# Kernel optimization log

Measured on AMD Instinct MI355X. Metric: run time of the kernel, lower is better.

The kernel has to match this reference:

```python
import jax, jax.numpy as jnp
import numpy as np

DIM = 1024
HEADS = 16
DIM_HEAD = 64
INNER = HEADS * DIM_HEAD
EPS_NORM = 1e-12  # F.normalize eps
LN_EPS = 1e-5     # torch F.layer_norm default eps


def setup_inputs() -> dict:
    key = jax.random.key(0)
    ks = jax.random.split(key, 6)
    x = jax.random.normal(ks[0], (8, 1024, DIM), dtype=jnp.float32)
    ln_gamma = jnp.ones((DIM,), jnp.float32)
    q_gamma = jnp.ones((HEADS, 1, DIM_HEAD), jnp.float32)
    k_gamma = jnp.ones((HEADS, 1, DIM_HEAD), jnp.float32)
    # nn.Linear default init ~ U(-1/sqrt(fan_in), 1/sqrt(fan_in))
    w_qkv = jax.random.uniform(ks[1], (DIM, 3 * INNER), jnp.float32, -1.0, 1.0) / np.sqrt(DIM)
    w_out = jax.random.uniform(ks[2], (INNER, DIM), jnp.float32, -1.0, 1.0) / np.sqrt(INNER)
    return {"x": x, "ln_gamma": ln_gamma, "q_gamma": q_gamma, "k_gamma": k_gamma,
            "w_qkv": w_qkv, "w_out": w_out}


def _layer_norm(x, gamma):
    mu = jnp.mean(x, axis=-1, keepdims=True)
    var = jnp.var(x, axis=-1, keepdims=True)
    return (x - mu) * jax.lax.rsqrt(var + LN_EPS) * gamma  # beta is zeros buffer


def _rms(x, gamma):
    # F.normalize(x, dim=-1) * sqrt(d) * gamma
    n = jnp.linalg.norm(x, axis=-1, keepdims=True)
    normed = x / jnp.maximum(n, EPS_NORM)
    return normed * (DIM_HEAD ** 0.5) * gamma


def reference(x, ln_gamma, q_gamma, k_gamma, w_qkv, w_out):
    b, n, _ = x.shape
    h, d = HEADS, DIM_HEAD
    xn = _layer_norm(x, ln_gamma)
    qkv = xn @ w_qkv  # [b, n, 3*inner]
    q, k, v = jnp.split(qkv, 3, axis=-1)
    # b n (h d) -> b h n d
    to_heads = lambda t: t.reshape(b, n, h, d).transpose(0, 2, 1, 3)
    q, k, v = to_heads(q), to_heads(k), to_heads(v)
    q = _rms(q, q_gamma)
    k = _rms(k, k_gamma)
    dots = jnp.einsum('bhid,bhjd->bhij', q, k)  # no extra scale (scale baked into RMSNorm)
    attn = jax.nn.softmax(dots, axis=-1)
    out = jnp.einsum('bhij,bhjd->bhid', attn, v)
    out = out.transpose(0, 2, 1, 3).reshape(b, n, h * d)
    return out @ w_out
```

## Files before the change

kernel.cpp:

```cpp
#include <hip/hip_runtime.h>
#include <hip/hip_bf16.h>
#include <math.h>

#define DIMX   1024
#define HEADS  16
#define DH     64
#define NB     8
#define NSEQ   1024
#define ROWS   (NB * NSEQ)
#define QKVW   (3 * DIMX)
#define LOG2E  1.44269504088896f

typedef _Float16 half8 __attribute__((ext_vector_type(8)));
typedef _Float16 half4 __attribute__((ext_vector_type(4)));
typedef float floatx4 __attribute__((ext_vector_type(4)));

#define GLD_LDS16(gptr, lptr) __builtin_amdgcn_global_load_lds( \
    (const __attribute__((address_space(1))) void*)(gptr),      \
    (__attribute__((address_space(3))) void*)(lptr), 16, 0, 0)

__device__ __forceinline__ float fexp2(float x) {
#if __has_builtin(__builtin_amdgcn_exp2f)
    return __builtin_amdgcn_exp2f(x);
#else
    return __expf(x * 0.69314718056f);
#endif
}

__global__ __launch_bounds__(256) void lnw_kernel(const float* __restrict__ x,
                                                  const float* __restrict__ gamma,
                                                  const float* __restrict__ Wq,
                                                  const float* __restrict__ Wo,
                                                  _Float16* __restrict__ xn,
                                                  _Float16* __restrict__ WqT,
                                                  _Float16* __restrict__ WoT) {
    __shared__ float tile[32][33];
    __shared__ float sbuf[4], ssbuf[4];
    int t = threadIdx.x;

    if (blockIdx.x < ROWS) {
        int row = blockIdx.x;
        const float* xr = x + (size_t)row * DIMX;
        _Float16* xo = xn + (size_t)row * DIMX;

        float4 v = ((const float4*)xr)[t];
        float s  = v.x + v.y + v.z + v.w;
        float ss = v.x*v.x + v.y*v.y + v.z*v.z + v.w*v.w;
        #pragma unroll
        for (int o = 32; o > 0; o >>= 1) {
            s  += __shfl_down(s, o);
            ss += __shfl_down(ss, o);
        }
        int lane = t & 63, wid = t >> 6;
        if (lane == 0) { sbuf[wid] = s; ssbuf[wid] = ss; }
        __syncthreads();
        if (t == 0) {
            float a = 0.f, b2 = 0.f;
            for (int i = 0; i < 4; i++) { a += sbuf[i]; b2 += ssbuf[i]; }
            sbuf[0] = a; ssbuf[0] = b2;
        }
        __syncthreads();
        float mean = sbuf[0] * (1.0f / DIMX);
        float var  = ssbuf[0] * (1.0f / DIMX) - mean * mean;
        float rstd = rsqrtf(var + 1e-5f);

        float4 g = ((const float4*)gamma)[t];
        half4 o;
        o.x = (_Float16)((v.x - mean) * rstd * g.x);
        o.y = (_Float16)((v.y - mean) * rstd * g.y);
        o.z = (_Float16)((v.z - mean) * rstd * g.z);
        o.w = (_Float16)((v.w - mean) * rstd * g.w);
        *(half4*)(xo + t * 4) = o;
    } else {
        int idx = blockIdx.x - ROWS;
        int bx = idx & 127, by = idx >> 7;
        const float* W; _Float16* WT; int N, n0;
        if (bx < 96) { W = Wq; WT = WqT; N = QKVW; n0 = bx * 32; }
        else         { W = Wo; WT = WoT; N = DIMX; n0 = (bx - 96) * 32; }
        int k0 = by * 32;
        int tx = t & 31, ty = t >> 5;
        #pragma unroll
        for (int i = 0; i < 32; i += 8)
            tile[ty + i][tx] = W[(size_t)(k0 + ty + i) * N + n0 + tx];
        __syncthreads();
        #pragma unroll
        for (int i = 0; i < 32; i += 8)
            WT[(size_t)(n0 + ty + i) * 1024 + k0 + tx] = (_Float16)tile[tx][ty + i];
    }
}

__global__ __launch_bounds__(256) void hgemm_qkv(const _Float16* __restrict__ A,
                                                 const _Float16* __restrict__ BT,
                                                 const float* __restrict__ qg,
                                                 const float* __restrict__ kg,
                                                 _Float16* __restrict__ qf,
                                                 _Float16* __restrict__ kf,
                                                 _Float16* __restrict__ vt) {
    __shared__ _Float16 As[128 * 64];
    __shared__ _Float16 Bs[128 * 64];
    const int K = DIMX;

    int t = threadIdx.x;
    int wave = t >> 6, lane = t & 63;
    int quad = lane >> 4, l16 = lane & 15;
    int wm = (wave >> 1) * 64;
    int wn = (wave & 1) * 64;
    size_t m0 = (size_t)blockIdx.y * 128, n0 = (size_t)blockIdx.x * 128;

    floatx4 acc[4][4] = {};

    int sr = t >> 3, sg = t & 7;
    int swz = sg ^ (sr & 7);
    const _Float16* ag = A  + (m0 + sr) * (size_t)K + swz * 8;
    const _Float16* bg = BT + (n0 + sr) * (size_t)K + swz * 8;
    char* lA = (char*)As + wave * 1024;
    char* lB = (char*)Bs + wave * 1024;

    for (int k0 = 0; k0 < K; k0 += 64) {
        #pragma unroll
        for (int i = 0; i < 4; i++) {
            GLD_LDS16(ag + (size_t)(i * 32) * K + k0, lA + i * 4096);
            GLD_LDS16(bg + (size_t)(i * 32) * K + k0, lB + i * 4096);
        }
        __syncthreads();

        half8 af[2][4], bf[2][4];
        #pragma unroll
        for (int kk = 0; kk < 2; kk++) {
            #pragma unroll
            for (int mf = 0; mf < 4; mf++)
                af[kk][mf] = *(const half8*)&As[(wm + mf * 16 + l16) * 64
                                 + (((kk * 4 + quad) ^ (l16 & 7)) * 8)];
            #pragma unroll
            for (int nf = 0; nf < 4; nf++)
                bf[kk][nf] = *(const half8*)&Bs[(wn + nf * 16 + l16) * 64
                                 + (((kk * 4 + quad) ^ (l16 & 7)) * 8)];
        }

        #pragma unroll
        for (int kk = 0; kk < 2; kk++)
            #pragma unroll
            for (int mf = 0; mf < 4; mf++)
                #pragma unroll
                for (int nf = 0; nf < 4; nf++)
                    acc[mf][nf] = __builtin_amdgcn_mfma_f32_16x16x32_f16(
                        bf[kk][nf], af[kk][mf], acc[mf][nf], 0, 0, 0);
        __syncthreads();
    }

    int which = (int)(n0 >> 10);
    int nloc  = ((int)n0 & 1023) + wn;
    int h = nloc >> 6;

    if (which < 2) {
        const float* g = (which == 0) ? qg : kg;
        float emul = (which == 0) ? LOG2E : 1.0f;
        _Float16* dstbuf = (which == 0) ? qf : kf;
        #pragma unroll
        for (int mf = 0; mf < 4; mf++) {
            size_t tok = m0 + wm + mf * 16 + l16;
            int b = (int)(tok >> 10), ntk = (int)(tok & 1023);
            _Float16* dst = dstbuf + (((size_t)(b * 16 + h)) * 1024 + ntk) * 64;
            float ss = 0.f;
            #pragma unroll
            for (int nf = 0; nf < 4; nf++)
                #pragma unroll
                for (int r = 0; r < 4; r++) ss += acc[mf][nf][r] * acc[mf][nf][r];
            ss += __shfl_xor(ss, 16);
            ss += __shfl_xor(ss, 32);
            float scale = 8.0f * emul / fmaxf(sqrtf(ss), 1e-12f);
            #pragma unroll
            for (int nf = 0; nf < 4; nf++) {
                half4 p;
                #pragma unroll
                for (int r = 0; r < 4; r++)
                    p[r] = (_Float16)(acc[mf][nf][r] * scale *
                                      g[h * 64 + nf * 16 + quad * 4 + r]);
                *(half4*)(dst + nf * 16 + quad * 4) = p;
            }
        }
    } else {
        #pragma unroll
        for (int mf = 0; mf < 4; mf++) {
            size_t tok = m0 + wm + mf * 16 + l16;
            int b = (int)(tok >> 10), ntk = (int)(tok & 1023);
            int nt = ntk >> 6;
            _Float16* vd = vt + ((size_t)((b * 16 + h) * 16 + nt) * 64) * 64
                              + mf * 16 + l16;
            #pragma unroll
            for (int nf = 0; nf < 4; nf++)
                #pragma unroll
                for (int r = 0; r < 4; r++)
                    vd[(size_t)(nf * 16 + quad * 4 + r) * 64] =
                        (_Float16)acc[mf][nf][r];
        }
    }
}

__global__ __launch_bounds__(256, 3) void flash_kernel(const _Float16* __restrict__ qf,
                                                       const _Float16* __restrict__ kf,
                                                       const _Float16* __restrict__ vt,
                                                       _Float16* __restrict__ obuf) {
    __shared__ _Float16 Ks[2][64 * 64];
    __shared__ _Float16 VTs[2][64 * 64];
    __shared__ _Float16 Ps[4][16][68];

    int t = threadIdx.x;
    int wave = t >> 6, lane = t & 63;
    int quad = lane >> 4, l16 = lane & 15;
    int bh = blockIdx.x & 127, qt = blockIdx.x >> 7;

    const _Float16* qb = qf + ((size_t)bh * 1024 + qt * 128) * 64;
    const _Float16* kb = kf + (size_t)bh * 65536;
    const _Float16* vb = vt + (size_t)bh * 65536;

    half8 aq[2][2];
    #pragma unroll
    for (int st = 0; st < 2; st++) {
        const _Float16* qrow = qb + (wave * 32 + st * 16 + l16) * 64;
        aq[st][0] = *(const half8*)(qrow + quad * 8);
        aq[st][1] = *(const half8*)(qrow + 32 + quad * 8);
    }

    floatx4 o[2][4] = {};
    float m_i[2] = {-INFINITY, -INFINITY};
    float l_i[2] = {0.f, 0.f};

    int sr = t >> 3;
    int sg = t & 7;
    int swz = sg ^ (sr & 7);

    #pragma unroll
    for (int i = 0; i < 2; i++) {
        GLD_LDS16(kb + (i * 32 + sr) * 64 + swz * 8, (char*)Ks[0]  + wave * 1024 + i * 4096);
        GLD_LDS16(vb + (i * 32 + sr) * 64 + swz * 8, (char*)VTs[0] + wave * 1024 + i * 4096);
    }

    for (int kt = 0; kt < 16; kt++) {
        int cur = kt & 1;
        __syncthreads();

        if (kt < 15) {
            const _Float16* kn = kb + (size_t)(kt + 1) * 4096;
            const _Float16* vn = vb + (size_t)(kt + 1) * 4096;
            #pragma unroll
            for (int i = 0; i < 2; i++) {
                GLD_LDS16(kn + (i * 32 + sr) * 64 + swz * 8,
                          (char*)Ks[cur ^ 1]  + wave * 1024 + i * 4096);
                GLD_LDS16(vn + (i * 32 + sr) * 64 + swz * 8,
                          (char*)VTs[cur ^ 1] + wave * 1024 + i * 4096);
            }
        }

        #pragma unroll
        for (int st = 0; st < 2; st++) {
            floatx4 sc[4] = {};
            #pragma unroll
            for (int kc = 0; kc < 2; kc++) {
                #pragma unroll
                for (int nf = 0; nf < 4; nf++) {
                    half8 ak = *(const half8*)&Ks[cur][(nf * 16 + l16) * 64
                                    + (((kc * 4 + quad) ^ (l16 & 7)) * 8)];
                    sc[nf] = __builtin_amdgcn_mfma_f32_16x16x32_f16(
                        ak, aq[st][kc], sc[nf], 0, 0, 0);
                }
            }

            float mx = sc[0][0];
            #pragma unroll
            for (int nf = 0; nf < 4; nf++)
                #pragma unroll
                for (int r = 0; r < 4; r++) mx = fmaxf(mx, sc[nf][r]);
            mx = fmaxf(mx, __shfl_xor(mx, 16));
            mx = fmaxf(mx, __shfl_xor(mx, 32));
            if (mx > m_i[st]) {
                float alpha = fexp2(m_i[st] - mx);
                l_i[st] *= alpha;
                #pragma unroll
                for (int nf = 0; nf < 4; nf++) o[st][nf] *= alpha;
                m_i[st] = mx;
            }
            float mcur = m_i[st];
            float psum = 0.f;
            #pragma unroll
            for (int nf = 0; nf < 4; nf++)
                #pragma unroll
                for (int r = 0; r < 4; r++) {
                    float p = fexp2(sc[nf][r] - mcur);
                    sc[nf][r] = p;
                    psum += p;
                }
            l_i[st] += psum;

            #pragma unroll
            for (int nf = 0; nf < 4; nf++) {
                half4 p4;
                #pragma unroll
                for (int r = 0; r < 4; r++) p4[r] = (_Float16)sc[nf][r];
                *(half4*)&Ps[wave][l16][nf * 16 + quad * 4] = p4;
            }

            #pragma unroll
            for (int kc = 0; kc < 2; kc++) {
                half4 p0 = *(const half4*)&Ps[wave][l16][kc * 32 + quad * 8];
                half4 p1 = *(const half4*)&Ps[wave][l16][kc * 32 + quad * 8 + 4];
                half8 bp;
                #pragma unroll
                for (int j = 0; j < 4; j++) { bp[j] = p0[j]; bp[4 + j] = p1[j]; }
                #pragma unroll
                for (int nf = 0; nf < 4; nf++) {
                    half8 av = *(const half8*)&VTs[cur][(nf * 16 + l16) * 64
                                    + (((kc * 4 + quad) ^ (l16 & 7)) * 8)];
                    o[st][nf] = __builtin_amdgcn_mfma_f32_16x16x32_f16(
                        av, bp, o[st][nf], 0, 0, 0);
                }
            }
        }
    }

    int b = bh >> 4, h = bh & 15;
    #pragma unroll
    for (int st = 0; st < 2; st++) {
        float lsum = l_i[st];
        lsum += __shfl_xor(lsum, 16);
        lsum += __shfl_xor(lsum, 32);
        float inv = 1.0f / lsum;
        size_t row = (size_t)b * NSEQ + qt * 128 + wave * 32 + st * 16 + l16;
        #pragma unroll
        for (int nf = 0; nf < 4; nf++) {
            half4 o4;
            #pragma unroll
            for (int r = 0; r < 4; r++) o4[r] = (_Float16)(o[st][nf][r] * inv);
            *(half4*)(obuf + row * 1024 + h * 64 + nf * 16 + quad * 4) = o4;
        }
    }
}

__global__ __launch_bounds__(256) void hgemm_out(const _Float16* __restrict__ A,
                                                 const _Float16* __restrict__ BT,
                                                 float* __restrict__ C) {
    __shared__ _Float16 As[128 * 64];
    __shared__ _Float16 Bs[128 * 64];
    const int K = DIMX, N = DIMX;

    int t = threadIdx.x;
    int wave = t >> 6, lane = t & 63;
    int quad = lane >> 4, l16 = lane & 15;
    int wm = (wave >> 1) * 64, wn = (wave & 1) * 64;
    size_t m0 = (size_t)blockIdx.y * 128, n0 = (size_t)blockIdx.x * 128;

    floatx4 acc[4][4] = {};

    int sr = t >> 3, sg = t & 7;
    int swz = sg ^ (sr & 7);
    const _Float16* ag = A  + (m0 + sr) * (size_t)K + swz * 8;
    const _Float16* bg = BT + (n0 + sr) * (size_t)K + swz * 8;
    char* lA = (char*)As + wave * 1024;
    char* lB = (char*)Bs + wave * 1024;

    for (int k0 = 0; k0 < K; k0 += 64) {
        #pragma unroll
        for (int i = 0; i < 4; i++) {
            GLD_LDS16(ag + (size_t)(i * 32) * K + k0, lA + i * 4096);
            GLD_LDS16(bg + (size_t)(i * 32) * K + k0, lB + i * 4096);
        }
        __syncthreads();

        half8 af[2][4], bf[2][4];
        #pragma unroll
        for (int kk = 0; kk < 2; kk++) {
            #pragma unroll
            for (int mf = 0; mf < 4; mf++)
                af[kk][mf] = *(const half8*)&As[(wm + mf * 16 + l16) * 64
                                 + (((kk * 4 + quad) ^ (l16 & 7)) * 8)];
            #pragma unroll
            for (int nf = 0; nf < 4; nf++)
                bf[kk][nf] = *(const half8*)&Bs[(wn + nf * 16 + l16) * 64
                                 + (((kk * 4 + quad) ^ (l16 & 7)) * 8)];
        }

        #pragma unroll
        for (int kk = 0; kk < 2; kk++)
            #pragma unroll
            for (int mf = 0; mf < 4; mf++)
                #pragma unroll
                for (int nf = 0; nf < 4; nf++)
                    acc[mf][nf] = __builtin_amdgcn_mfma_f32_16x16x32_f16(
                        bf[kk][nf], af[kk][mf], acc[mf][nf], 0, 0, 0);
        __syncthreads();
    }

    #pragma unroll
    for (int mf = 0; mf < 4; mf++) {
        size_t tok = m0 + wm + mf * 16 + l16;
        #pragma unroll
        for (int nf = 0; nf < 4; nf++)
            *(floatx4*)(C + tok * N + n0 + wn + nf * 16 + quad * 4) = acc[mf][nf];
    }
}

extern "C" void kernel_launch(void* const* d_in, const int* in_sizes, int n_in,
                              void* d_out, int out_size, void* d_ws, size_t ws_size,
                              hipStream_t stream) {
    const float* x     = (const float*)d_in[0];
    const float* ln_g  = (const float*)d_in[1];
    const float* q_g   = (const float*)d_in[2];
    const float* k_g   = (const float*)d_in[3];
    const float* w_qkv = (const float*)d_in[4];
    const float* w_out = (const float*)d_in[5];
    float* out = (float*)d_out;

    char* base = (char*)d_ws;
    _Float16* xn    = (_Float16*)(base);
    _Float16* wqkvT = (_Float16*)(base + (16ull << 20));
    _Float16* woutT = (_Float16*)(base + (22ull << 20));
    _Float16* qf    = (_Float16*)(base + (24ull << 20));
    _Float16* kf    = (_Float16*)(base + (40ull << 20));
    _Float16* vt    = (_Float16*)(base + (56ull << 20));
    _Float16* obuf  = (_Float16*)(base + (72ull << 20));

    lnw_kernel<<<ROWS + 4096, 256, 0, stream>>>(x, ln_g, w_qkv, w_out,
                                                xn, wqkvT, woutT);

    dim3 g1(QKVW / 128, ROWS / 128);
    hgemm_qkv<<<g1, 256, 0, stream>>>(xn, wqkvT, q_g, k_g, qf, kf, vt);

    flash_kernel<<<NB * HEADS * (NSEQ / 128), 256, 0, stream>>>(qf, kf, vt, obuf);

    dim3 g2(DIMX / 128, ROWS / 128);
    hgemm_out<<<g2, 256, 0, stream>>>(obuf, woutT, out);
}
```

Baseline: 260.0 us.

## Add 256x128-tile QKV GEMM with 4-stage async LDS pipeline

```diff
diff --git a/kernel.cpp b/kernel.cpp
--- a/kernel.cpp
+++ b/kernel.cpp
@@ -89,13 +89,136 @@
     }
 }
 
-__global__ __launch_bounds__(256) void hgemm_qkv(const _Float16* __restrict__ A,
-                                                 const _Float16* __restrict__ BT,
-                                                 const float* __restrict__ qg,
-                                                 const float* __restrict__ kg,
-                                                 _Float16* __restrict__ qf,
-                                                 _Float16* __restrict__ kf,
-                                                 _Float16* __restrict__ vt) {
+__global__ __launch_bounds__(512, 2) void hgemm_qkv_big(const _Float16* __restrict__ A,
+                                                        const _Float16* __restrict__ BT,
+                                                        const float* __restrict__ qg,
+                                                        const float* __restrict__ kg,
+                                                        _Float16* __restrict__ qf,
+                                                        _Float16* __restrict__ kf,
+                                                        _Float16* __restrict__ vt) {
+    extern __shared__ char smem[];
+    const int K = DIMX;
+
+    int t = threadIdx.x;
+    int wave = t >> 6, lane = t & 63;
+    int quad = lane >> 4, l16 = lane & 15;
+    int wm = (wave >> 1) * 64;
+    int wn = (wave & 1) * 64;
+    size_t m0 = (size_t)blockIdx.y * 256, n0 = (size_t)blockIdx.x * 128;
+
+    floatx4 acc[4][4] = {};
+
+    int lr = lane >> 2;
+    int ksw = (lane & 3) ^ ((lane >> 3) & 3);
+    const _Float16* ag = A  + (m0 + wave * 32 + lr) * (size_t)K + ksw * 8;
+    const _Float16* bg = BT + (n0 + wave * 16 + lr) * (size_t)K + ksw * 8;
+    int rsw = (l16 >> 1) & 3;
+
+#define STAGE(s) do { int _sb = (int)(s) & 3; size_t _ko = (size_t)(s) * 32;    \
+        char* _bb = smem + _sb * 24576;                                         \
+        GLD_LDS16(ag + _ko,          _bb + wave * 2048);                        \
+        GLD_LDS16(ag + 16 * K + _ko, _bb + wave * 2048 + 1024);                 \
+        GLD_LDS16(bg + _ko,          _bb + 16384 + wave * 1024);                \
+    } while (0)
+
+#define STEP_BODY(s, STAGE_STMT, WAIT_STMT) do {                                \
+        int _rb = (int)(s) & 3;                                                 \
+        const _Float16* As_ = (const _Float16*)(smem + _rb * 24576);            \
+        const _Float16* Bs_ = (const _Float16*)(smem + _rb * 24576 + 16384);    \
+        STAGE_STMT;                                                             \
+        half8 af[4], bf[4];                                                     \
+        _Pragma("unroll")                                                       \
+        for (int mf = 0; mf < 4; mf++)                                          \
+            af[mf] = *(const half8*)&As_[(wm + mf * 16 + l16) * 32              \
+                                         + (quad ^ rsw) * 8];                   \
+        _Pragma("unroll")                                                       \
+        for (int nf = 0; nf < 4; nf++)                                          \
+            bf[nf] = *(const half8*)&Bs_[(wn + nf * 16 + l16) * 32              \
+                                         + (quad ^ rsw) * 8];                   \
+        __builtin_amdgcn_s_setprio(1);                                          \
+        _Pragma("unroll")                                                       \
+        for (int mf = 0; mf < 4; mf++)                                          \
+            _Pragma("unroll")                                                   \
+            for (int nf = 0; nf < 4; nf++)                                      \
+                acc[mf][nf] = __builtin_amdgcn_mfma_f32_16x16x32_f16(           \
+                    bf[nf], af[mf], acc[mf][nf], 0, 0, 0);                      \
+        __builtin_amdgcn_s_setprio(0);                                          \
+        WAIT_STMT;                                                              \
+        __builtin_amdgcn_s_barrier();                                           \
+        asm volatile("" ::: "memory");                                          \
+    } while (0)
+
+    STAGE(0); STAGE(1); STAGE(2);
+    asm volatile("s_waitcnt vmcnt(6)" ::: "memory");
+    __builtin_amdgcn_s_barrier();
+    asm volatile("" ::: "memory");
+
+    for (int s = 0; s < 29; s++)
+        STEP_BODY(s, STAGE(s + 3),
+                  asm volatile("s_waitcnt vmcnt(6)" ::: "memory"));
+    STEP_BODY(29, ((void)0), asm volatile("s_waitcnt vmcnt(3)" ::: "memory"));
+    STEP_BODY(30, ((void)0), asm volatile("s_waitcnt vmcnt(0)" ::: "memory"));
+    STEP_BODY(31, ((void)0), ((void)0));
+
+#undef STAGE
+#undef STEP_BODY
+
+    int which = (int)(n0 >> 10);
+    int nloc  = ((int)n0 & 1023) + wn;
+    int h = nloc >> 6;
+
+    if (which < 2) {
+        const float* g = (which == 0) ? qg : kg;
+        float emul = (which == 0) ? LOG2E : 1.0f;
+        _Float16* dstbuf = (which == 0) ? qf : kf;
+        #pragma unroll
+        for (int mf = 0; mf < 4; mf++) {
+            size_t tok = m0 + wm + mf * 16 + l16;
+            int b = (int)(tok >> 10), ntk = (int)(tok & 1023);
+            _Float16* dst = dstbuf + (((size_t)(b * 16 + h)) * 1024 + ntk) * 64;
+            float ss = 0.f;
+            #pragma unroll
+            for (int nf = 0; nf < 4; nf++)
+                #pragma unroll
+                for (int r = 0; r < 4; r++) ss += acc[mf][nf][r] * acc[mf][nf][r];
+            ss += __shfl_xor(ss, 16);
+            ss += __shfl_xor(ss, 32);
+            float scale = 8.0f * emul / fmaxf(sqrtf(ss), 1e-12f);
+            #pragma unroll
+            for (int nf = 0; nf < 4; nf++) {
+                half4 p;
+                #pragma unroll
+                for (int r = 0; r < 4; r++)
+                    p[r] = (_Float16)(acc[mf][nf][r] * scale *
+                                      g[h * 64 + nf * 16 + quad * 4 + r]);
+                *(half4*)(dst + nf * 16 + quad * 4) = p;
+            }
+        }
+    } else {
+        #pragma unroll
+        for (int mf = 0; mf < 4; mf++) {
+            size_t tok = m0 + wm + mf * 16 + l16;
+            int b = (int)(tok >> 10), ntk = (int)(tok & 1023);
+            int nt = ntk >> 6;
+            _Float16* vd = vt + ((size_t)((b * 16 + h) * 16 + nt) * 64) * 64
+                              + mf * 16 + l16;
+            #pragma unroll
+            for (int nf = 0; nf < 4; nf++)
+                #pragma unroll
+                for (int r = 0; r < 4; r++)
+                    vd[(size_t)(nf * 16 + quad * 4 + r) * 64] =
+                        (_Float16)acc[mf][nf][r];
+        }
+    }
+}
+
+__global__ __launch_bounds__(256) void hgemm_qkv_small(const _Float16* __restrict__ A,
+                                                       const _Float16* __restrict__ BT,
+                                                       const float* __restrict__ qg,
+                                                       const float* __restrict__ kg,
+                                                       _Float16* __restrict__ qf,
+                                                       _Float16* __restrict__ kf,
+                                                       _Float16* __restrict__ vt) {
     __shared__ _Float16 As[128 * 64];
     __shared__ _Float16 Bs[128 * 64];
     const int K = DIMX;
@@ -419,11 +542,30 @@
     _Float16* vt    = (_Float16*)(base + (56ull << 20));
     _Float16* obuf  = (_Float16*)(base + (72ull << 20));
 
+    static int use_big = -1;
+    if (use_big < 0) {
+        int ok = 0;
+        if (hipFuncSetAttribute((const void*)hgemm_qkv_big,
+                                hipFuncAttributeMaxDynamicSharedMemorySize,
+                                98304) == hipSuccess) {
+            hipFuncAttributes fa;
+            if (hipFuncGetAttributes(&fa, (const void*)hgemm_qkv_big) == hipSuccess
+                && fa.maxDynamicSharedSizeBytes >= 98304)
+                ok = 1;
+        }
+        use_big = ok;
+    }
+
     lnw_kernel<<<ROWS + 4096, 256, 0, stream>>>(x, ln_g, w_qkv, w_out,
                                                 xn, wqkvT, woutT);
 
-    dim3 g1(QKVW / 128, ROWS / 128);
-    hgemm_qkv<<<g1, 256, 0, stream>>>(xn, wqkvT, q_g, k_g, qf, kf, vt);
+    if (use_big) {
+        dim3 g1(QKVW / 128, ROWS / 256);
+        hgemm_qkv_big<<<g1, 512, 98304, stream>>>(xn, wqkvT, q_g, k_g, qf, kf, vt);
+    } else {
+        dim3 g1(QKVW / 128, ROWS / 128);
+        hgemm_qkv_small<<<g1, 256, 0, stream>>>(xn, wqkvT, q_g, k_g, qf, kf, vt);
+    }
 
     flash_kernel<<<NB * HEADS * (NSEQ / 128), 256, 0, stream>>>(qf, kf, vt, obuf);
 
```

Result: slower. 265.6 us (+2.2%).
